# Performance work log

Measured on AMD Instinct MI355X. Metric: run time of the kernel, lower is better.

Reference implementation:

```python
import jax, jax.numpy as jnp
import numpy as np

D_MODEL = 1024
NUM_HEADS = 16
DEPTH = D_MODEL // NUM_HEADS
MAX_REL_POS = 128


def setup_inputs() -> dict:
    key = jax.random.key(0)
    ks = jax.random.split(key, 12)
    B, S = 2, 2048
    inp = {
        "q": jax.random.normal(ks[0], (B, S, D_MODEL), jnp.float32),
        "k": jax.random.normal(ks[1], (B, S, D_MODEL), jnp.float32),
        "v": jax.random.normal(ks[2], (B, S, D_MODEL), jnp.float32),
        "mask": jnp.zeros((B, 1, 1, S), jnp.float32),
        "wq": jax.random.normal(ks[3], (D_MODEL, D_MODEL), jnp.float32) * (D_MODEL ** -0.5),
        "bq": jnp.zeros((D_MODEL,), jnp.float32),
        "wk": jax.random.normal(ks[4], (D_MODEL, D_MODEL), jnp.float32) * (D_MODEL ** -0.5),
        "bk": jnp.zeros((D_MODEL,), jnp.float32),
        "wv": jax.random.normal(ks[5], (D_MODEL, D_MODEL), jnp.float32) * (D_MODEL ** -0.5),
        "bv": jnp.zeros((D_MODEL,), jnp.float32),
        "wo": jax.random.normal(ks[6], (D_MODEL, D_MODEL), jnp.float32) * (D_MODEL ** -0.5),
        "bo": jnp.zeros((D_MODEL,), jnp.float32),
        "rel_k_emb": jax.random.normal(ks[7], (2 * MAX_REL_POS + 1, DEPTH), jnp.float32) * 0.02,
        "rel_v_emb": jax.random.normal(ks[8], (2 * MAX_REL_POS + 1, DEPTH), jnp.float32) * 0.02,
    }
    return inp


def _split_heads(x, B):
    # [B, S, d_model] -> [B, H, S, depth]
    S = x.shape[1]
    return x.reshape(B, S, NUM_HEADS, DEPTH).transpose(0, 2, 1, 3)


def reference(q, k, v, mask, wq, bq, wk, bk, wv, bv, wo, bo, rel_k_emb, rel_v_emb):
    B, S, _ = q.shape
    qh = _split_heads(q @ wq + bq, B)  # [B,H,S,d]
    kh = _split_heads(k @ wk + bk, B)
    vh = _split_heads(v @ wv + bv, B)

    # relative position indices [S, S] in [0, 2*MAX_REL_POS]
    ar = jnp.arange(S)
    dist = jnp.clip(ar[None, :] - ar[:, None], -MAX_REL_POS, MAX_REL_POS) + MAX_REL_POS
    rk = rel_k_emb[dist]  # [S, S, depth]
    rv = rel_v_emb[dist]  # [S, S, depth]

    logits = jnp.einsum("bhqd,bhkd->bhqk", qh, kh)
    logits = logits + jnp.einsum("bhqd,qkd->bhqk", qh, rk)
    logits = logits * (1.0 / jnp.sqrt(jnp.float32(DEPTH)))
    logits = logits + mask * -1e9
    attn = jax.nn.softmax(logits, axis=-1)  # [B,H,Sq,Sk]

    out = jnp.einsum("bhqk,bhkd->bhqd", attn, vh)
    out = out + jnp.einsum("bhqk,qkd->bhqd", attn, rv)

    out = out.transpose(0, 2, 1, 3).reshape(B, S, D_MODEL)
    out = out @ wo + bo
    return out, attn
```

## Files before the change

kernel.cpp:

```cpp
#include <hip/hip_runtime.h>
#include <hip/hip_bf16.h>
#include <cstdint>
#include <cstddef>

#define DM   1024
#define NH   16
#define DH   64
#define SEQ  2048
#define BB   2
#define NREL 257
#define BHN  (BB*NH)
#define ROWS (BB*SEQ)

typedef __attribute__((ext_vector_type(8))) short bf16x8;
typedef __attribute__((ext_vector_type(4))) float f32x4;
typedef __attribute__((ext_vector_type(8))) unsigned short us8;
typedef __attribute__((ext_vector_type(4))) unsigned short us4;

__device__ __forceinline__ unsigned short f2bf(float x){
  union { float f; unsigned u; } v; v.f = x;
  unsigned r = v.u + 0x7fffu + ((v.u >> 16) & 1u);
  return (unsigned short)(r >> 16);
}
__device__ __forceinline__ float b2f(unsigned short h){
  union { unsigned u; float f; } v; v.u = ((unsigned)h) << 16;
  return v.f;
}

__device__ __forceinline__ void gload_lds16(const void* g, void* l){
  __builtin_amdgcn_global_load_lds((const __attribute__((address_space(1))) unsigned int*)g,
                                   (__attribute__((address_space(3))) unsigned int*)l, 16, 0, 0);
}


__global__ void k_cast(const float* __restrict__ x, unsigned short* __restrict__ o, int n4){
  int i = blockIdx.x*blockDim.x + threadIdx.x;
  int st = gridDim.x*blockDim.x;
  for (; i < n4; i += st){
    float4 f = ((const float4*)x)[i];
    us4 v = { f2bf(f.x), f2bf(f.y), f2bf(f.z), f2bf(f.w) };
    *(us4*)(o + (size_t)i*4) = v;
  }
}

__global__ void k_wtrans(const float* __restrict__ W, unsigned short* __restrict__ T){
  __shared__ float t[64][65];
  int k0 = blockIdx.x*64, n0 = blockIdx.y*64;
  int tid = threadIdx.x;
  for (int u = tid; u < 4096; u += 256){
    int r = u >> 6, c = u & 63;
    t[r][c] = W[(size_t)(k0+r)*DM + n0 + c];
  }
  __syncthreads();
  for (int u = tid; u < 4096; u += 256){
    int r = u >> 6, c = u & 63;
    T[(size_t)(n0+r)*DM + k0 + c] = f2bf(t[c][r]);
  }
}

__global__ void k_embk(const float* __restrict__ e, unsigned short* __restrict__ eb){
  int i = blockIdx.x*256 + threadIdx.x;
  if (i >= 272*64) return;
  int r = i >> 6;
  float v = e[min(i, NREL*64 - 1)];
  eb[i] = (r < NREL) ? f2bf(v) : (unsigned short)0;
}

__global__ void k_embt(const float* __restrict__ rv, unsigned short* __restrict__ embT){
  int i = blockIdx.x*256 + threadIdx.x;
  if (i >= 64*256) return;
  int d = i >> 8, j = i & 255;
  float v = rv[(size_t)min(j+1, 256)*DH + d];
  embT[i] = (j < 255) ? f2bf(v) : (unsigned short)0;
}

__launch_bounds__(256, 2)
__global__ void k_proj(const unsigned short* __restrict__ A, const unsigned short* __restrict__ Bt,
                       const float* __restrict__ bias, unsigned short* __restrict__ O){
  __shared__ __align__(16) unsigned short sm[2*4096];
  const int tid = threadIdx.x;
  const int w = tid >> 6, lane = tid & 63;
  const int m0 = (blockIdx.x >> 3) * 128;
  const int n0 = (blockIdx.x & 7) * 128;
  const int wr = (w >> 1) * 64, wc = (w & 1) * 64;
  const int fr = lane & 15, fo = (lane >> 4)*8, fq = (lane >> 4)*4;
  f32x4 acc[4][4] = {};
  for (int k0 = 0; k0 < DM; k0 += 32){
    const unsigned short* srcs[2] = { A + (size_t)m0*DM + k0, Bt + (size_t)n0*DM + k0 };
#pragma unroll
    for (int t = 0; t < 2; ++t)
#pragma unroll
      for (int p = 0; p < 2; ++p){
        int o = p*4096 + tid*16;
        int row = o >> 6, cb = o & 63;
        const char* g = (const char*)(srcs[t] + (size_t)row*DM) + cb;
        char* l = ((char*)sm) + t*8192 + o;
        gload_lds16(g, l);
      }
    __syncthreads();
    bf16x8 af[4], bf[4];
#pragma unroll
    for (int i = 0; i < 4; ++i){
      af[i] = *(const bf16x8*)&sm[0*4096 + (wr + i*16 + fr)*32 + fo];
      bf[i] = *(const bf16x8*)&sm[1*4096 + (wc + i*16 + fr)*32 + fo];
    }
#pragma unroll
    for (int i = 0; i < 4; ++i)
#pragma unroll
      for (int j = 0; j < 4; ++j)
        acc[i][j] = __builtin_amdgcn_mfma_f32_16x16x32_bf16(af[i], bf[j], acc[i][j], 0,0,0);
    __syncthreads();
  }
#pragma unroll
  for (int i = 0; i < 4; ++i)
#pragma unroll
    for (int j = 0; j < 4; ++j){
      int col = n0 + wc + j*16 + fr;
      float bs = bias[col];
      int h = col >> 6, d = col & 63;
#pragma unroll
      for (int r = 0; r < 4; ++r){
        int row = m0 + wr + i*16 + fq + r;
        int b = row >> 11, s = row & 2047;
        O[((size_t)(b*NH + h)*SEQ + s)*DH + d] = f2bf(acc[i][j][r] + bs);
      }
    }
}

__global__ void k_vtrans(const unsigned short* __restrict__ vh, unsigned short* __restrict__ vt){
  __shared__ __align__(16) unsigned short t[64][72];
  int bh = blockIdx.x >> 5, st = blockIdx.x & 31;
  int s0 = st*64;
  int tid = threadIdx.x;
#pragma unroll
  for (int p = 0; p < 2; ++p){
    int u = tid + p*256;
    int row = u >> 3, ch = u & 7;
    *(us8*)&t[row][ch*8] = *(const us8*)(vh + ((size_t)bh*SEQ + s0 + row)*DH + ch*8);
  }
  __syncthreads();
#pragma unroll
  for (int p = 0; p < 2; ++p){
    int u = tid + p*256;
    int dr = u >> 3, ch = u & 7;
    us8 v;
#pragma unroll
    for (int j = 0; j < 8; ++j) v[j] = t[ch*8+j][dr];
    *(us8*)(vt + ((size_t)bh*DH + dr)*SEQ + s0 + ch*8) = v;
  }
}

__launch_bounds__(256, 2)
__global__ void k_attn(const unsigned short* __restrict__ qh, const unsigned short* __restrict__ kh,
                       const unsigned short* __restrict__ vt, const unsigned short* __restrict__ embk,
                       const float* __restrict__ mask,
                       unsigned short* __restrict__ Pb, float* __restrict__ Zout,
                       float* __restrict__ ctxu){
  __shared__ unsigned short qrl[64*NREL];
  __shared__ __align__(16) unsigned short Kh[64][72], Vt[64][72], Pl[64][72];
  __shared__ float mls[SEQ];

  const int tid = threadIdx.x, w = tid >> 6, lane = tid & 63;
  const int bh = blockIdx.x >> 5, qt = blockIdx.x & 31;
  const int b = bh >> 4;
  const int q0 = qt * 64;
  const int fr = lane & 15, fo = (lane >> 4) * 8, fq = (lane >> 4) * 4;

  for (int i = tid; i < SEQ; i += 256) mls[i] = mask[b*SEQ + i] * (-1e9f);

  bf16x8 q_hi[2];
  {
    size_t base = ((size_t)bh*SEQ + q0 + w*16 + fr) * DH;
#pragma unroll
    for (int ks = 0; ks < 2; ++ks)
      q_hi[ks] = *(const bf16x8*)(qh + base + ks*32 + fo);
  }

#pragma unroll 1
  for (int jt = 0; jt < 17; ++jt){
    f32x4 a = {};
#pragma unroll
    for (int ks = 0; ks < 2; ++ks){
      bf16x8 e = *(const bf16x8*)(embk + ((size_t)(jt*16 + fr))*DH + ks*32 + fo);
      a = __builtin_amdgcn_mfma_f32_16x16x32_bf16(q_hi[ks], e, a, 0,0,0);
    }
    int rr = jt*16 + fr;
#pragma unroll
    for (int r = 0; r < 4; ++r){
      if (rr < NREL) qrl[(w*16 + fq + r)*NREL + rr] = f2bf(a[r]);
    }
  }
  float rcL[4], rcR[4];
#pragma unroll
  for (int r = 0; r < 4; ++r){
    int ql = w*16 + fq + r;
    rcL[r] = b2f(qrl[ql*NREL + 0])   * 0.125f;
    rcR[r] = b2f(qrl[ql*NREL + 256]) * 0.125f;
  }

  const unsigned short* kb = kh + (size_t)bh*SEQ*DH;
  const unsigned short* vb = vt + (size_t)bh*DH*SEQ;

  const int srow = tid >> 3, sch = (tid & 7) * 8;
  us8 rKh[2], rVt[2];
  auto issue = [&](int kt){
#pragma unroll
    for (int p = 0; p < 2; ++p){
      int row = srow + p*32;
      rKh[p] = *(const us8*)(kb + ((size_t)(kt*64 + row))*DH + sch);
      rVt[p] = *(const us8*)(vb + ((size_t)row)*SEQ + kt*64 + sch);
    }
  };
  auto commit = [&](){
#pragma unroll
    for (int p = 0; p < 2; ++p){
      int row = srow + p*32;
      *(us8*)&Kh[row][sch] = rKh[p];
      *(us8*)&Vt[row][sch] = rVt[p];
    }
  };

  float zpart[4] = {0.f,0.f,0.f,0.f};
  f32x4 ctx[4] = {};

  issue(0); commit();
  __syncthreads();

#pragma unroll 1
  for (int kt = 0; kt < 32; ++kt){
    if (kt < 31) issue(kt + 1);

    const bool leftU  = (kt*64 + 191) <= q0;
    const bool rightU = (kt*64) >= (q0 + 191);

    float pv[4][4];
#pragma unroll
    for (int c = 0; c < 4; ++c){
      f32x4 a = {};
#pragma unroll
      for (int ks = 0; ks < 2; ++ks){
        bf16x8 kf = *(const bf16x8*)&Kh[c*16 + fr][ks*32 + fo];
        a = __builtin_amdgcn_mfma_f32_16x16x32_bf16(q_hi[ks], kf, a, 0,0,0);
      }
      int kg = kt*64 + c*16 + fr;
      float mv = mls[kg];
      if (leftU){
#pragma unroll
        for (int r = 0; r < 4; ++r)
          pv[c][r] = __expf(a[r]*0.125f + rcL[r] + mv);
      } else if (rightU){
#pragma unroll
        for (int r = 0; r < 4; ++r)
          pv[c][r] = __expf(a[r]*0.125f + rcR[r] + mv);
      } else {
#pragma unroll
        for (int r = 0; r < 4; ++r){
          int ql = w*16 + fq + r;
          int qg = q0 + ql;
          int dd = kg - qg; dd = min(max(dd, -128), 128);
          float rel = b2f(qrl[ql*NREL + dd + 128]);
          pv[c][r] = __expf((a[r] + rel)*0.125f + mv);
        }
      }
    }
#pragma unroll
    for (int r = 0; r < 4; ++r)
      zpart[r] += pv[0][r] + pv[1][r] + pv[2][r] + pv[3][r];
#pragma unroll
    for (int c = 0; c < 4; ++c)
#pragma unroll
      for (int r = 0; r < 4; ++r)
        Pl[w*16 + fq + r][c*16 + fr] = f2bf(pv[c][r]);
    {
      int lr = lane >> 2, ch = lane & 3;
      const unsigned short* src = &Pl[w*16 + lr][0];
      size_t gbase = ((size_t)bh*SEQ + q0 + w*16 + lr)*SEQ + kt*64;
      *(us8*)(Pb + gbase + ch*8)     = *(const us8*)(src + ch*8);
      *(us8*)(Pb + gbase + (ch+4)*8) = *(const us8*)(src + (ch+4)*8);
    }
#pragma unroll
    for (int ks = 0; ks < 2; ++ks){
      bf16x8 pf = *(const bf16x8*)&Pl[w*16 + fr][ks*32 + fo];
#pragma unroll
      for (int j = 0; j < 4; ++j){
        bf16x8 vf = *(const bf16x8*)&Vt[j*16 + fr][ks*32 + fo];
        ctx[j] = __builtin_amdgcn_mfma_f32_16x16x32_bf16(pf, vf, ctx[j], 0,0,0);
      }
    }
    if (kt < 31){
      __syncthreads();
      commit();
      __syncthreads();
    }
  }

#pragma unroll
  for (int r = 0; r < 4; ++r){
    float part = zpart[r];
    part += __shfl_xor(part, 1);
    part += __shfl_xor(part, 2);
    part += __shfl_xor(part, 4);
    part += __shfl_xor(part, 8);
    zpart[r] = part;
  }
  if (fr == 0){
#pragma unroll
    for (int r = 0; r < 4; ++r)
      Zout[(size_t)bh*SEQ + q0 + w*16 + fq + r] = zpart[r];
  }
#pragma unroll
  for (int j = 0; j < 4; ++j)
#pragma unroll
    for (int r = 0; r < 4; ++r)
      ctxu[((size_t)bh*SEQ + q0 + w*16 + fq + r)*DH + j*16 + fr] = ctx[j][r];
}

__launch_bounds__(256, 4)
__global__ void k_norm(const unsigned short* __restrict__ Pb, float* __restrict__ attn,
                       const float* __restrict__ Z,
                       const float* __restrict__ ctxu, const unsigned short* __restrict__ embT,
                       const float* __restrict__ rv, unsigned short* __restrict__ ctxb){
  __shared__ __align__(16) unsigned short band[64*256];
  __shared__ float invr[64], Lr[64], Rr[64];
  const int tid = threadIdx.x, w = tid >> 6, lane = tid & 63;
  const int bh = blockIdx.x >> 5, qt = blockIdx.x & 31;
  const int q0 = qt * 64;
  const int fr = lane & 15, fo = (lane >> 4) * 8, fq = (lane >> 4) * 4;

  {
    us8 z = {0,0,0,0,0,0,0,0};
    for (int i = tid; i < 64*256/8; i += 256) ((us8*)band)[i] = z;
  }
  __syncthreads();

#pragma unroll 1
  for (int rr = 0; rr < 16; ++rr){
    int rl = w*16 + rr;
    int q = q0 + rl;
    size_t R = (size_t)bh*SEQ + q;
    float inv = 1.0f / Z[R];
    float la = 0.f, ra = 0.f;
    const us8* prow = (const us8*)(Pb + R*SEQ);
    float4* orow = (float4*)(attn + R*SEQ);
    unsigned short* brow = band + rl*256;
    const int sw = (rl & 7) << 3;
#pragma unroll 1
    for (int c = 0; c < 4; ++c){
      us8 p8 = prow[c*64 + lane];
      float pe[8];
#pragma unroll
      for (int e = 0; e < 8; ++e) pe[e] = b2f(p8[e]);
      float4 o0 = {pe[0]*inv, pe[1]*inv, pe[2]*inv, pe[3]*inv};
      float4 o1 = {pe[4]*inv, pe[5]*inv, pe[6]*inv, pe[7]*inv};
      orow[(c*64 + lane)*2]     = o0;
      orow[(c*64 + lane)*2 + 1] = o1;
      int jlo = c*512 - q + 127;
      if (jlo + 511 < 0){
        la += pe[0]+pe[1]+pe[2]+pe[3]+pe[4]+pe[5]+pe[6]+pe[7];
      } else if (jlo > 254){
        ra += pe[0]+pe[1]+pe[2]+pe[3]+pe[4]+pe[5]+pe[6]+pe[7];
      } else {
        int jb = jlo + lane*8;
#pragma unroll
        for (int e = 0; e < 8; ++e){
          int j = jb + e;
          if (j < 0)        la += pe[e];
          else if (j > 254) ra += pe[e];
          else              brow[j ^ sw] = p8[e];
        }
      }
    }
#pragma unroll
    for (int m = 1; m < 64; m <<= 1){
      la += __shfl_xor(la, m);
      ra += __shfl_xor(ra, m);
    }
    if (lane == 0){ invr[rl] = inv; Lr[rl] = la; Rr[rl] = ra; }
  }
  __syncthreads();

  f32x4 acc[4] = {};
  {
    const int arow = w*16 + fr;
    const int asw = (arow & 7) << 3;
    const unsigned short* bandr = band + arow*256;
#pragma unroll
    for (int kk = 0; kk < 8; ++kk){
      bf16x8 af = *(const bf16x8*)&bandr[(kk*32 + fo) ^ asw];
#pragma unroll
      for (int jt = 0; jt < 4; ++jt){
        bf16x8 bfr = *(const bf16x8*)(embT + (size_t)(jt*16 + fr)*256 + kk*32 + fo);
        acc[jt] = __builtin_amdgcn_mfma_f32_16x16x32_bf16(af, bfr, acc[jt], 0,0,0);
      }
    }
  }

  const int b = bh >> 4, h = bh & 15;
#pragma unroll
  for (int jt = 0; jt < 4; ++jt){
    int d = jt*16 + fr;
    float e0 = rv[d], e256 = rv[(size_t)256*DH + d];
#pragma unroll
    for (int r = 0; r < 4; ++r){
      int rl = w*16 + fq + r;
      int q = q0 + rl;
      float cv = (ctxu[((size_t)bh*SEQ + q)*DH + d] + acc[jt][r] + Lr[rl]*e0 + Rr[rl]*e256) * invr[rl];
      ctxb[((size_t)b*SEQ + q)*DM + h*DH + d] = f2bf(cv);
    }
  }
}

__launch_bounds__(256, 2)
__global__ void k_out(const unsigned short* __restrict__ A, const unsigned short* __restrict__ Bt,
                      const float* __restrict__ bias, float* __restrict__ out){
  __shared__ __align__(16) unsigned short sm[2*4096];
  const int tid = threadIdx.x;
  const int w = tid >> 6, lane = tid & 63;
  const int m0 = (blockIdx.x >> 3) * 128;
  const int n0 = (blockIdx.x & 7) * 128;
  const int wr = (w >> 1) * 64, wc = (w & 1) * 64;
  const int fr = lane & 15, fo = (lane >> 4)*8, fq = (lane >> 4)*4;
  f32x4 acc[4][4] = {};
  for (int k0 = 0; k0 < DM; k0 += 32){
    const unsigned short* srcs[2] = { A + (size_t)m0*DM + k0, Bt + (size_t)n0*DM + k0 };
#pragma unroll
    for (int t = 0; t < 2; ++t)
#pragma unroll
      for (int p = 0; p < 2; ++p){
        int o = p*4096 + tid*16;
        int row = o >> 6, cb = o & 63;
        const char* g = (const char*)(srcs[t] + (size_t)row*DM) + cb;
        char* l = ((char*)sm) + t*8192 + o;
        gload_lds16(g, l);
      }
    __syncthreads();
    bf16x8 af[4], bf[4];
#pragma unroll
    for (int i = 0; i < 4; ++i){
      af[i] = *(const bf16x8*)&sm[0*4096 + (wr + i*16 + fr)*32 + fo];
      bf[i] = *(const bf16x8*)&sm[1*4096 + (wc + i*16 + fr)*32 + fo];
    }
#pragma unroll
    for (int i = 0; i < 4; ++i)
#pragma unroll
      for (int j = 0; j < 4; ++j)
        acc[i][j] = __builtin_amdgcn_mfma_f32_16x16x32_bf16(af[i], bf[j], acc[i][j], 0,0,0);
    __syncthreads();
  }
#pragma unroll
  for (int i = 0; i < 4; ++i)
#pragma unroll
    for (int j = 0; j < 4; ++j){
      int col = n0 + wc + j*16 + fr;
      float bs = bias[col];
#pragma unroll
      for (int r = 0; r < 4; ++r){
        int row = m0 + wr + i*16 + fq + r;
        out[(size_t)row*DM + col] = acc[i][j][r] + bs;
      }
    }
}

extern "C" void kernel_launch(void* const* d_in, const int* in_sizes, int n_in,
                              void* d_out, int out_size, void* d_ws, size_t ws_size,
                              hipStream_t stream){
  const float* q    = (const float*)d_in[0];
  const float* k    = (const float*)d_in[1];
  const float* v    = (const float*)d_in[2];
  const float* mask = (const float*)d_in[3];
  const float* wq   = (const float*)d_in[4];
  const float* bq   = (const float*)d_in[5];
  const float* wk   = (const float*)d_in[6];
  const float* bk   = (const float*)d_in[7];
  const float* wv   = (const float*)d_in[8];
  const float* bv   = (const float*)d_in[9];
  const float* wo   = (const float*)d_in[10];
  const float* bo   = (const float*)d_in[11];
  const float* rk   = (const float*)d_in[12];
  const float* rv   = (const float*)d_in[13];

  float* out  = (float*)d_out;
  float* attn = out + (size_t)ROWS*DM;

  char* p = (char*)d_ws;
  size_t used = 0;
  auto alloc = [&](size_t bytes) -> char* {
    char* r = p;
    size_t a = (bytes + 255) & ~(size_t)255;
    p += a; used += a;
    return r;
  };
  const size_t NE  = (size_t)ROWS*DM;
  unsigned short* qb   = (unsigned short*)alloc(NE*2);
  unsigned short* kbf  = (unsigned short*)alloc(NE*2);
  unsigned short* vbf  = (unsigned short*)alloc(NE*2);
  unsigned short* wqt  = (unsigned short*)alloc((size_t)DM*DM*2);
  unsigned short* wkt  = (unsigned short*)alloc((size_t)DM*DM*2);
  unsigned short* wvt  = (unsigned short*)alloc((size_t)DM*DM*2);
  unsigned short* wot  = (unsigned short*)alloc((size_t)DM*DM*2);
  unsigned short* qh   = (unsigned short*)alloc(NE*2);
  unsigned short* kh   = (unsigned short*)alloc(NE*2);
  unsigned short* vh   = (unsigned short*)alloc(NE*2);
  unsigned short* vht  = (unsigned short*)alloc(NE*2);
  unsigned short* embk = (unsigned short*)alloc((size_t)272*64*2);
  unsigned short* embT = (unsigned short*)alloc((size_t)64*256*2);
  float* Zb   = (float*)alloc((size_t)BHN*SEQ*4);
  float* ctxu = (float*)alloc((size_t)BHN*SEQ*DH*4);
  unsigned short* ctxb = (unsigned short*)alloc(NE*2);
  unsigned short* Pb   = (unsigned short*)alloc((size_t)BHN*SEQ*SEQ*2);
  if (used > ws_size) return;

  const int N4 = (int)(NE/4);
  k_cast<<<2048, 256, 0, stream>>>(q, qb, N4);
  k_cast<<<2048, 256, 0, stream>>>(k, kbf, N4);
  k_cast<<<2048, 256, 0, stream>>>(v, vbf, N4);
  dim3 tg(16,16);
  k_wtrans<<<tg, 256, 0, stream>>>(wq, wqt);
  k_wtrans<<<tg, 256, 0, stream>>>(wk, wkt);
  k_wtrans<<<tg, 256, 0, stream>>>(wv, wvt);
  k_wtrans<<<tg, 256, 0, stream>>>(wo, wot);
  k_embk<<<(272*64+255)/256, 256, 0, stream>>>(rk, embk);
  k_embt<<<64, 256, 0, stream>>>(rv, embT);

  k_proj<<<256, 256, 0, stream>>>(qb,  wqt, bq, qh);
  k_proj<<<256, 256, 0, stream>>>(kbf, wkt, bk, kh);
  k_proj<<<256, 256, 0, stream>>>(vbf, wvt, bv, vh);
  k_vtrans<<<1024, 256, 0, stream>>>(vh, vht);

  k_attn<<<1024, 256, 0, stream>>>(qh, kh, vht, embk, mask, Pb, Zb, ctxu);
  k_norm<<<1024, 256, 0, stream>>>(Pb, attn, Zb, ctxu, embT, rv, ctxb);
  k_out<<<256, 256, 0, stream>>>(ctxb, wot, bo, out);
}
```

Before: 511.5 us.

## Split attention into Z pass and normalized PV pass, drop bf16 P buffer

Replaces the single attention kernel, which wrote an unnormalized bf16 P matrix, with two passes. A cheap pass computes only the softmax denominators. A second pass recomputes the logits, writes the normalized fp32 attn directly, computes PV, and accumulates the clipped left and right edge sums. The relative-position kernel now reads only the band of attn, instead of streaming the whole P buffer and rewriting attn. This removes the 256MB bf16 round trip at the cost of recomputing QK^T and exp twice. The attn stores in the PV pass are strided and narrow, which may coalesce poorly.

```diff
diff --git a/kernel.cpp b/kernel.cpp
--- a/kernel.cpp
+++ b/kernel.cpp
@@ -150,14 +150,12 @@
   }
 }
 
-__launch_bounds__(256, 2)
-__global__ void k_attn(const unsigned short* __restrict__ qh, const unsigned short* __restrict__ kh,
-                       const unsigned short* __restrict__ vt, const unsigned short* __restrict__ embk,
-                       const float* __restrict__ mask,
-                       unsigned short* __restrict__ Pb, float* __restrict__ Zout,
-                       float* __restrict__ ctxu){
+__launch_bounds__(256, 3)
+__global__ void k_attnZ(const unsigned short* __restrict__ qh, const unsigned short* __restrict__ kh,
+                        const unsigned short* __restrict__ embk, const float* __restrict__ mask,
+                        float* __restrict__ Zout){
   __shared__ unsigned short qrl[64*NREL];
-  __shared__ __align__(16) unsigned short Kh[64][72], Vt[64][72], Pl[64][72];
+  __shared__ __align__(16) unsigned short Kh[64][72];
   __shared__ float mls[SEQ];
 
   const int tid = threadIdx.x, w = tid >> 6, lane = tid & 63;
@@ -199,41 +197,28 @@
   }
 
   const unsigned short* kb = kh + (size_t)bh*SEQ*DH;
-  const unsigned short* vb = vt + (size_t)bh*DH*SEQ;
-
   const int srow = tid >> 3, sch = (tid & 7) * 8;
-  us8 rKh[2], rVt[2];
+  us8 rKh[2];
   auto issue = [&](int kt){
 #pragma unroll
-    for (int p = 0; p < 2; ++p){
-      int row = srow + p*32;
-      rKh[p] = *(const us8*)(kb + ((size_t)(kt*64 + row))*DH + sch);
-      rVt[p] = *(const us8*)(vb + ((size_t)row)*SEQ + kt*64 + sch);
-    }
+    for (int p = 0; p < 2; ++p)
+      rKh[p] = *(const us8*)(kb + ((size_t)(kt*64 + srow + p*32))*DH + sch);
   };
   auto commit = [&](){
 #pragma unroll
-    for (int p = 0; p < 2; ++p){
-      int row = srow + p*32;
-      *(us8*)&Kh[row][sch] = rKh[p];
-      *(us8*)&Vt[row][sch] = rVt[p];
-    }
+    for (int p = 0; p < 2; ++p)
+      *(us8*)&Kh[srow + p*32][sch] = rKh[p];
   };
 
   float zpart[4] = {0.f,0.f,0.f,0.f};
-  f32x4 ctx[4] = {};
-
   issue(0); commit();
   __syncthreads();
 
 #pragma unroll 1
   for (int kt = 0; kt < 32; ++kt){
     if (kt < 31) issue(kt + 1);
-
     const bool leftU  = (kt*64 + 191) <= q0;
     const bool rightU = (kt*64) >= (q0 + 191);
-
-    float pv[4][4];
 #pragma unroll
     for (int c = 0; c < 4; ++c){
       f32x4 a = {};
@@ -246,12 +231,10 @@
       float mv = mls[kg];
       if (leftU){
 #pragma unroll
-        for (int r = 0; r < 4; ++r)
-          pv[c][r] = __expf(a[r]*0.125f + rcL[r] + mv);
+        for (int r = 0; r < 4; ++r) zpart[r] += __expf(a[r]*0.125f + rcL[r] + mv);
       } else if (rightU){
 #pragma unroll
-        for (int r = 0; r < 4; ++r)
-          pv[c][r] = __expf(a[r]*0.125f + rcR[r] + mv);
+        for (int r = 0; r < 4; ++r) zpart[r] += __expf(a[r]*0.125f + rcR[r] + mv);
       } else {
 #pragma unroll
         for (int r = 0; r < 4; ++r){
@@ -259,32 +242,8 @@
           int qg = q0 + ql;
           int dd = kg - qg; dd = min(max(dd, -128), 128);
           float rel = b2f(qrl[ql*NREL + dd + 128]);
-          pv[c][r] = __expf((a[r] + rel)*0.125f + mv);
+          zpart[r] += __expf((a[r] + rel)*0.125f + mv);
         }
-      }
-    }
-#pragma unroll
-    for (int r = 0; r < 4; ++r)
-      zpart[r] += pv[0][r] + pv[1][r] + pv[2][r] + pv[3][r];
-#pragma unroll
-    for (int c = 0; c < 4; ++c)
-#pragma unroll
-      for (int r = 0; r < 4; ++r)
-        Pl[w*16 + fq + r][c*16 + fr] = f2bf(pv[c][r]);
-    {
-      int lr = lane >> 2, ch = lane & 3;
-      const unsigned short* src = &Pl[w*16 + lr][0];
-      size_t gbase = ((size_t)bh*SEQ + q0 + w*16 + lr)*SEQ + kt*64;
-      *(us8*)(Pb + gbase + ch*8)     = *(const us8*)(src + ch*8);
-      *(us8*)(Pb + gbase + (ch+4)*8) = *(const us8*)(src + (ch+4)*8);
-    }
-#pragma unroll
-    for (int ks = 0; ks < 2; ++ks){
-      bf16x8 pf = *(const bf16x8*)&Pl[w*16 + fr][ks*32 + fo];
-#pragma unroll
-      for (int j = 0; j < 4; ++j){
-        bf16x8 vf = *(const bf16x8*)&Vt[j*16 + fr][ks*32 + fo];
-        ctx[j] = __builtin_amdgcn_mfma_f32_16x16x32_bf16(pf, vf, ctx[j], 0,0,0);
       }
     }
     if (kt < 31){
@@ -308,6 +267,174 @@
     for (int r = 0; r < 4; ++r)
       Zout[(size_t)bh*SEQ + q0 + w*16 + fq + r] = zpart[r];
   }
+}
+
+__launch_bounds__(256, 2)
+__global__ void k_attnPV(const unsigned short* __restrict__ qh, const unsigned short* __restrict__ kh,
+                         const unsigned short* __restrict__ vt, const unsigned short* __restrict__ embk,
+                         const float* __restrict__ mask, const float* __restrict__ Zb,
+                         float* __restrict__ attn, float* __restrict__ ctxu,
+                         float* __restrict__ Lb, float* __restrict__ Rb){
+  __shared__ unsigned short qrl[64*NREL];
+  __shared__ __align__(16) unsigned short Kh[64][72], Vt[64][72], Pl[64][72];
+  __shared__ float mls[SEQ];
+
+  const int tid = threadIdx.x, w = tid >> 6, lane = tid & 63;
+  const int bh = blockIdx.x >> 5, qt = blockIdx.x & 31;
+  const int b = bh >> 4;
+  const int q0 = qt * 64;
+  const int fr = lane & 15, fo = (lane >> 4) * 8, fq = (lane >> 4) * 4;
+
+  for (int i = tid; i < SEQ; i += 256) mls[i] = mask[b*SEQ + i] * (-1e9f);
+
+  bf16x8 q_hi[2];
+  {
+    size_t base = ((size_t)bh*SEQ + q0 + w*16 + fr) * DH;
+#pragma unroll
+    for (int ks = 0; ks < 2; ++ks)
+      q_hi[ks] = *(const bf16x8*)(qh + base + ks*32 + fo);
+  }
+
+#pragma unroll 1
+  for (int jt = 0; jt < 17; ++jt){
+    f32x4 a = {};
+#pragma unroll
+    for (int ks = 0; ks < 2; ++ks){
+      bf16x8 e = *(const bf16x8*)(embk + ((size_t)(jt*16 + fr))*DH + ks*32 + fo);
+      a = __builtin_amdgcn_mfma_f32_16x16x32_bf16(q_hi[ks], e, a, 0,0,0);
+    }
+    int rr = jt*16 + fr;
+#pragma unroll
+    for (int r = 0; r < 4; ++r){
+      if (rr < NREL) qrl[(w*16 + fq + r)*NREL + rr] = f2bf(a[r]);
+    }
+  }
+  float rcL[4], rcR[4], inv[4];
+#pragma unroll
+  for (int r = 0; r < 4; ++r){
+    int ql = w*16 + fq + r;
+    rcL[r] = b2f(qrl[ql*NREL + 0])   * 0.125f;
+    rcR[r] = b2f(qrl[ql*NREL + 256]) * 0.125f;
+    inv[r] = 1.0f / Zb[(size_t)bh*SEQ + q0 + ql];
+  }
+
+  const unsigned short* kb = kh + (size_t)bh*SEQ*DH;
+  const unsigned short* vb = vt + (size_t)bh*DH*SEQ;
+
+  const int srow = tid >> 3, sch = (tid & 7) * 8;
+  us8 rKh[2], rVt[2];
+  auto issue = [&](int kt){
+#pragma unroll
+    for (int p = 0; p < 2; ++p){
+      int row = srow + p*32;
+      rKh[p] = *(const us8*)(kb + ((size_t)(kt*64 + row))*DH + sch);
+      rVt[p] = *(const us8*)(vb + ((size_t)row)*SEQ + kt*64 + sch);
+    }
+  };
+  auto commit = [&](){
+#pragma unroll
+    for (int p = 0; p < 2; ++p){
+      int row = srow + p*32;
+      *(us8*)&Kh[row][sch] = rKh[p];
+      *(us8*)&Vt[row][sch] = rVt[p];
+    }
+  };
+
+  float la[4] = {0.f,0.f,0.f,0.f}, ra[4] = {0.f,0.f,0.f,0.f};
+  f32x4 ctx[4] = {};
+
+  issue(0); commit();
+  __syncthreads();
+
+#pragma unroll 1
+  for (int kt = 0; kt < 32; ++kt){
+    if (kt < 31) issue(kt + 1);
+
+    const bool leftU  = (kt*64 + 191) <= q0;
+    const bool rightU = (kt*64) >= (q0 + 191);
+
+    float pn[4][4];
+#pragma unroll
+    for (int c = 0; c < 4; ++c){
+      f32x4 a = {};
+#pragma unroll
+      for (int ks = 0; ks < 2; ++ks){
+        bf16x8 kf = *(const bf16x8*)&Kh[c*16 + fr][ks*32 + fo];
+        a = __builtin_amdgcn_mfma_f32_16x16x32_bf16(q_hi[ks], kf, a, 0,0,0);
+      }
+      int kg = kt*64 + c*16 + fr;
+      float mv = mls[kg];
+      if (leftU){
+#pragma unroll
+        for (int r = 0; r < 4; ++r){
+          float p = __expf(a[r]*0.125f + rcL[r] + mv) * inv[r];
+          pn[c][r] = p; la[r] += p;
+        }
+      } else if (rightU){
+#pragma unroll
+        for (int r = 0; r < 4; ++r){
+          float p = __expf(a[r]*0.125f + rcR[r] + mv) * inv[r];
+          pn[c][r] = p; ra[r] += p;
+        }
+      } else {
+#pragma unroll
+        for (int r = 0; r < 4; ++r){
+          int ql = w*16 + fq + r;
+          int qg = q0 + ql;
+          int dd = kg - qg;
+          int dc = min(max(dd, -128), 128);
+          float rel = b2f(qrl[ql*NREL + dc + 128]);
+          float p = __expf((a[r] + rel)*0.125f + mv) * inv[r];
+          pn[c][r] = p;
+          if (dd <= -128)     la[r] += p;
+          else if (dd >= 128) ra[r] += p;
+        }
+      }
+      {
+        size_t rowb = ((size_t)bh*SEQ + q0 + w*16 + fq) * SEQ + kg;
+#pragma unroll
+        for (int r = 0; r < 4; ++r)
+          attn[rowb + (size_t)r*SEQ] = pn[c][r];
+      }
+    }
+#pragma unroll
+    for (int c = 0; c < 4; ++c)
+#pragma unroll
+      for (int r = 0; r < 4; ++r)
+        Pl[w*16 + fq + r][c*16 + fr] = f2bf(pn[c][r]);
+#pragma unroll
+    for (int ks = 0; ks < 2; ++ks){
+      bf16x8 pf = *(const bf16x8*)&Pl[w*16 + fr][ks*32 + fo];
+#pragma unroll
+      for (int j = 0; j < 4; ++j){
+        bf16x8 vf = *(const bf16x8*)&Vt[j*16 + fr][ks*32 + fo];
+        ctx[j] = __builtin_amdgcn_mfma_f32_16x16x32_bf16(pf, vf, ctx[j], 0,0,0);
+      }
+    }
+    if (kt < 31){
+      __syncthreads();
+      commit();
+      __syncthreads();
+    }
+  }
+
+#pragma unroll
+  for (int r = 0; r < 4; ++r){
+    float pl = la[r], pr = ra[r];
+    pl += __shfl_xor(pl, 1); pr += __shfl_xor(pr, 1);
+    pl += __shfl_xor(pl, 2); pr += __shfl_xor(pr, 2);
+    pl += __shfl_xor(pl, 4); pr += __shfl_xor(pr, 4);
+    pl += __shfl_xor(pl, 8); pr += __shfl_xor(pr, 8);
+    la[r] = pl; ra[r] = pr;
+  }
+  if (fr == 0){
+#pragma unroll
+    for (int r = 0; r < 4; ++r){
+      size_t R = (size_t)bh*SEQ + q0 + w*16 + fq + r;
+      Lb[R] = la[r];
+      Rb[R] = ra[r];
+    }
+  }
 #pragma unroll
   for (int j = 0; j < 4; ++j)
 #pragma unroll
@@ -316,12 +443,11 @@
 }
 
 __launch_bounds__(256, 4)
-__global__ void k_norm(const unsigned short* __restrict__ Pb, float* __restrict__ attn,
-                       const float* __restrict__ Z,
-                       const float* __restrict__ ctxu, const unsigned short* __restrict__ embT,
-                       const float* __restrict__ rv, unsigned short* __restrict__ ctxb){
+__global__ void k_rel(const float* __restrict__ attn, const float* __restrict__ ctxu,
+                      const unsigned short* __restrict__ embT, const float* __restrict__ rv,
+                      const float* __restrict__ Lb, const float* __restrict__ Rb,
+                      unsigned short* __restrict__ ctxb){
   __shared__ __align__(16) unsigned short band[64*256];
-  __shared__ float invr[64], Lr[64], Rr[64];
   const int tid = threadIdx.x, w = tid >> 6, lane = tid & 63;
   const int bh = blockIdx.x >> 5, qt = blockIdx.x & 31;
   const int q0 = qt * 64;
@@ -338,44 +464,16 @@
     int rl = w*16 + rr;
     int q = q0 + rl;
     size_t R = (size_t)bh*SEQ + q;
-    float inv = 1.0f / Z[R];
-    float la = 0.f, ra = 0.f;
-    const us8* prow = (const us8*)(Pb + R*SEQ);
-    float4* orow = (float4*)(attn + R*SEQ);
+    int j0 = (q >= 127)  ? 0   : (127 - q);
+    int j1 = (q <= 1920) ? 254 : (2174 - q);
+    const int sw = (rl & 7) << 3;
     unsigned short* brow = band + rl*256;
-    const int sw = (rl & 7) << 3;
-#pragma unroll 1
-    for (int c = 0; c < 4; ++c){
-      us8 p8 = prow[c*64 + lane];
-      float pe[8];
-#pragma unroll
-      for (int e = 0; e < 8; ++e) pe[e] = b2f(p8[e]);
-      float4 o0 = {pe[0]*inv, pe[1]*inv, pe[2]*inv, pe[3]*inv};
-      float4 o1 = {pe[4]*inv, pe[5]*inv, pe[6]*inv, pe[7]*inv};
-      orow[(c*64 + lane)*2]     = o0;
-      orow[(c*64 + lane)*2 + 1] = o1;
-      int jlo = c*512 - q + 127;
-      if (jlo + 511 < 0){
-        la += pe[0]+pe[1]+pe[2]+pe[3]+pe[4]+pe[5]+pe[6]+pe[7];
-      } else if (jlo > 254){
-        ra += pe[0]+pe[1]+pe[2]+pe[3]+pe[4]+pe[5]+pe[6]+pe[7];
-      } else {
-        int jb = jlo + lane*8;
-#pragma unroll
-        for (int e = 0; e < 8; ++e){
-          int j = jb + e;
-          if (j < 0)        la += pe[e];
-          else if (j > 254) ra += pe[e];
-          else              brow[j ^ sw] = p8[e];
-        }
-      }
-    }
-#pragma unroll
-    for (int m = 1; m < 64; m <<= 1){
-      la += __shfl_xor(la, m);
-      ra += __shfl_xor(ra, m);
-    }
-    if (lane == 0){ invr[rl] = inv; Lr[rl] = la; Rr[rl] = ra; }
+#pragma unroll
+    for (int e = 0; e < 4; ++e){
+      int j = lane*4 + e;
+      if (j >= j0 && j <= j1)
+        brow[j ^ sw] = f2bf(attn[R*SEQ + (size_t)(q + j - 127)]);
+    }
   }
   __syncthreads();
 
@@ -404,7 +502,8 @@
     for (int r = 0; r < 4; ++r){
       int rl = w*16 + fq + r;
       int q = q0 + rl;
-      float cv = (ctxu[((size_t)bh*SEQ + q)*DH + d] + acc[jt][r] + Lr[rl]*e0 + Rr[rl]*e256) * invr[rl];
+      size_t R = (size_t)bh*SEQ + q;
+      float cv = ctxu[R*DH + d] + acc[jt][r] + Lb[R]*e0 + Rb[R]*e256;
       ctxb[((size_t)b*SEQ + q)*DM + h*DH + d] = f2bf(cv);
     }
   }
@@ -505,9 +604,10 @@
   unsigned short* embk = (unsigned short*)alloc((size_t)272*64*2);
   unsigned short* embT = (unsigned short*)alloc((size_t)64*256*2);
   float* Zb   = (float*)alloc((size_t)BHN*SEQ*4);
+  float* Lb   = (float*)alloc((size_t)BHN*SEQ*4);
+  float* Rb   = (float*)alloc((size_t)BHN*SEQ*4);
   float* ctxu = (float*)alloc((size_t)BHN*SEQ*DH*4);
   unsigned short* ctxb = (unsigned short*)alloc(NE*2);
-  unsigned short* Pb   = (unsigned short*)alloc((size_t)BHN*SEQ*SEQ*2);
   if (used > ws_size) return;
 
   const int N4 = (int)(NE/4);
@@ -527,7 +627,8 @@
   k_proj<<<256, 256, 0, stream>>>(vbf, wvt, bv, vh);
   k_vtrans<<<1024, 256, 0, stream>>>(vh, vht);
 
-  k_attn<<<1024, 256, 0, stream>>>(qh, kh, vht, embk, mask, Pb, Zb, ctxu);
-  k_norm<<<1024, 256, 0, stream>>>(Pb, attn, Zb, ctxu, embT, rv, ctxb);
+  k_attnZ<<<1024, 256, 0, stream>>>(qh, kh, embk, mask, Zb);
+  k_attnPV<<<1024, 256, 0, stream>>>(qh, kh, vht, embk, mask, Zb, attn, ctxu, Lb, Rb);
+  k_rel<<<1024, 256, 0, stream>>>(attn, ctxu, embT, rv, Lb, Rb, ctxb);
   k_out<<<256, 256, 0, stream>>>(ctxb, wot, bo, out);
 }
```

After: 527.8 us. 3.2% more time.
